# Performance work log

Hardware: AMD Instinct MI355X
Metric: run time of the kernel (lower is better)

Reference implementation:

```python
import jax, jax.numpy as jnp
import numpy as np

K = 1024          # num_embeddings
D = 64            # embedding_dim
TEMP = 1.0        # cfg.temperature
EPS = 1e-10


def setup_inputs() -> dict:
    key = jax.random.key(0)
    k1, k2 = jax.random.split(key)
    return {
        "inputs": jax.random.normal(k1, (16, 2048, D), dtype=jnp.float32),
        "embedding": jax.random.normal(k2, (K, D), dtype=jnp.float32),
        "code_count": jnp.ones((K,), dtype=jnp.float32),
    }


def _distances(flat, embedding):
    return ((flat ** 2).sum(axis=1, keepdims=True)
            + (embedding ** 2).sum(axis=1)
            - 2.0 * flat @ embedding.T)


def reference(inputs, embedding, code_count):
    B = inputs.shape[0]
    flat = inputs.reshape(-1, D)                      # [N, D]
    N = flat.shape[0]

    d = _distances(flat, embedding)                   # [N, K]
    idx = jnp.argmin(d, axis=1)                       # [N]

    # one-hot @ codebook == gather by index
    quantized = embedding[idx].reshape(inputs.shape)

    commitment_loss = jnp.mean((jax.lax.stop_gradient(quantized) - inputs) ** 2)

    # ortho loss over used codes (code_count >= 1), via masking (jit-safe)
    mask = (code_count >= 1.0).astype(inputs.dtype)   # [K]
    n_used = mask.sum()
    normed = embedding / jnp.clip(
        jnp.linalg.norm(embedding, axis=1, keepdims=True), 1e-12)
    normed = normed * mask[:, None]                   # zero out unused rows
    cos = normed @ normed.T                           # [K, K]
    ortho_loss = (cos ** 2).sum() / (n_used ** 2) - 1.0 / n_used

    # entropy loss over softmax(-d / T)
    prob = jax.nn.softmax(-d / TEMP, axis=1)          # [N, K]
    entropy_loss = -jnp.mean(jnp.sum(prob * jnp.log(prob + EPS), axis=1))
    entropy_loss = entropy_loss / jnp.log2(jnp.asarray(K, inputs.dtype))

    # straight-through estimator
    quantized_st = inputs + jax.lax.stop_gradient(quantized - inputs)

    # perplexity from code usage histogram (mean of one-hot encodings)
    avg_probs = jnp.zeros((K,), inputs.dtype).at[idx].add(1.0) / N
    perplexity = jnp.exp(-jnp.sum(avg_probs * jnp.log(avg_probs + EPS)))

    coverage = mask.sum() / K
    indices = idx.reshape(B, -1)

    return (quantized_st, commitment_loss, ortho_loss, entropy_loss,
            perplexity, coverage, indices)
```

## Files before the change

### kernel.cpp

```cpp
#include <hip/hip_runtime.h>
#include <math.h>

#define N_ROWS  32768
#define K_CODES 1024
#define D_DIM   64
#define NSPLIT  4
#define C_SHIFT 30.0f
#define LOG2E_F 1.4426950408889634f
#define LN2_F   0.6931471805599453f

#define WS_HIST   0
#define WS_ACC_H  1024
#define WS_ACC_C  1025
#define WS_NUSED  1026
#define WS_G      2048
#define WS_E2C    6144
#define PART_STRIDE (NSPLIT * N_ROWS)
#define WS_PART_S  8192
#define WS_PART_U  (8192 + PART_STRIDE)
#define WS_PART_AB (8192 + 2 * PART_STRIDE)
#define WS_EB      (8192 + 3 * PART_STRIDE)
#define CHUNK_F4  260
#define MAIN_CHUNKS 16
#define MEMSET_BYTES (6144 * 4)

#define OUT_Q      0
#define OUT_COMMIT 2097152
#define OUT_ORTHO  2097153
#define OUT_ENT    2097154
#define OUT_PERP   2097155
#define OUT_COV    2097156
#define OUT_IDX    2097157

typedef __attribute__((ext_vector_type(8))) _Float16 f16x8;
typedef __attribute__((ext_vector_type(4))) float f32x4;

__device__ inline float exact_g(const float4* X, const float* __restrict__ emb,
                                int k, float e2ck) {
    const float4* e4 = (const float4*)(emb + (size_t)k * D_DIM);
    float d0 = 0.f, d1 = 0.f, d2 = 0.f, d3 = 0.f;
#pragma unroll
    for (int j = 0; j < 16; j += 4) {
        float4 ea = e4[j], eb = e4[j + 1], ec = e4[j + 2], ed = e4[j + 3];
        float4 xa = X[j], xb = X[j + 1], xc = X[j + 2], xd = X[j + 3];
        d0 = fmaf(ea.x, xa.x, d0); d0 = fmaf(ea.y, xa.y, d0);
        d0 = fmaf(ea.z, xa.z, d0); d0 = fmaf(ea.w, xa.w, d0);
        d1 = fmaf(eb.x, xb.x, d1); d1 = fmaf(eb.y, xb.y, d1);
        d1 = fmaf(eb.z, xb.z, d1); d1 = fmaf(eb.w, xb.w, d1);
        d2 = fmaf(ec.x, xc.x, d2); d2 = fmaf(ec.y, xc.y, d2);
        d2 = fmaf(ec.z, xc.z, d2); d2 = fmaf(ec.w, xc.w, d2);
        d3 = fmaf(ed.x, xd.x, d3); d3 = fmaf(ed.y, xd.y, d3);
        d3 = fmaf(ed.z, xd.z, d3); d3 = fmaf(ed.w, xd.w, d3);
    }
    return fmaf(2.0f, (d0 + d1) + (d2 + d3), -e2ck);
}

__device__ inline void decomp2x8(const float* v, f16x8& h, f16x8& m) {
#pragma unroll
    for (int i = 0; i < 8; ++i) {
        _Float16 hh = (_Float16)v[i];
        h[i] = hh;
        m[i] = (_Float16)(v[i] - (float)hh);
    }
}

__global__ __launch_bounds__(256) void vq_prep_ortho(const float* __restrict__ emb,
                                                     const float* __restrict__ cc,
                                                     float* __restrict__ ws) {
    __shared__ float srows[64][64];
    __shared__ float rn2[64];
    const int t = threadIdx.x;

    if (blockIdx.x < 16) {
        const int tid  = blockIdx.x * 256 + t;
        const int c    = tid >> 6;
        const int lane = tid & 63;
        const int col  = lane & 15;
        const int kg   = lane >> 4;
        const int code = c * 16 + col;
        float4* EB4 = (float4*)(ws + WS_EB);
#pragma unroll
        for (int s = 0; s < 2; ++s) {
            const float* ep = emb + (size_t)code * D_DIM + s * 32 + kg * 8;
            float4 A4 = *(const float4*)ep;
            float4 B4 = *(const float4*)(ep + 4);
            float v[8] = {A4.x, A4.y, A4.z, A4.w, B4.x, B4.y, B4.z, B4.w};
            union { f16x8 h; float4 f; } th, tm;
            decomp2x8(v, th.h, tm.h);
            const int base = c * CHUNK_F4;
            EB4[base + (s * 2 + 0) * 64 + lane] = th.f;
            EB4[base + (s * 2 + 1) * 64 + lane] = tm.f;
        }
        if (kg == 0) {
            const float4* e4 = (const float4*)(emb + (size_t)code * D_DIM);
            float ssum = 0.f;
#pragma unroll
            for (int j = 0; j < 16; ++j) {
                float4 v = e4[j];
                ssum += v.x * v.x + v.y * v.y + v.z * v.z + v.w * v.w;
            }
            float e2c = ssum + C_SHIFT;
            ws[WS_E2C + code] = e2c;
            ((float*)(EB4 + c * CHUNK_F4 + 256))[col] = e2c * LOG2E_F;
            if (cc[code] >= 1.0f) atomicAdd(&ws[WS_NUSED], 1.0f);
        }
        return;
    }

    const int k0 = (blockIdx.x - 16) * 64;
    const int rb = t >> 4;
    const int c4 = (t & 15) << 2;

#pragma unroll
    for (int i = 0; i < 4; ++i) {
        const int r = i * 16 + rb;
        float4 v = *(const float4*)(emb + (size_t)(k0 + r) * D_DIM + c4);
        *(float4*)(&srows[r][c4]) = v;
        float ss = v.x * v.x + v.y * v.y + v.z * v.z + v.w * v.w;
        ss += __shfl_down(ss, 8, 16);
        ss += __shfl_down(ss, 4, 16);
        ss += __shfl_down(ss, 2, 16);
        ss += __shfl_down(ss, 1, 16);
        if ((t & 15) == 0) {
            float nrm = fmaxf(sqrtf(ss), 1e-12f);
            float m = (cc[k0 + r] >= 1.0f) ? 1.0f : 0.0f;
            rn2[r] = m / (nrm * nrm);
        }
    }
    __syncthreads();

    const int a  = t >> 2;
    const int b0 = (t & 3) << 4;
    float acc[16];
#pragma unroll
    for (int i = 0; i < 16; ++i) acc[i] = 0.f;

#pragma unroll 4
    for (int k = 0; k < 64; ++k) {
        float na = srows[k][a] * rn2[k];
        const float* rbp = &srows[k][b0];
#pragma unroll
        for (int i = 0; i < 16; ++i) acc[i] = fmaf(na, rbp[i], acc[i]);
    }
#pragma unroll
    for (int i = 0; i < 16; ++i)
        atomicAdd(&ws[WS_G + a * 64 + b0 + i], acc[i]);
}

#define MFMA_F16 __builtin_amdgcn_mfma_f32_16x16x32_f16

__global__ __launch_bounds__(256)
__attribute__((amdgpu_waves_per_eu(4, 4)))
void vq_main(const float* __restrict__ inp, float* __restrict__ ws) {
    const int t    = threadIdx.x;
    const int lane = t & 63;
    const int wave = t >> 6;
    const int col  = lane & 15;
    const int kg   = lane >> 4;
    const int rg   = blockIdx.x >> 2;
    const int sp   = blockIdx.x & 3;
    const int wbase = rg * 128 + wave * 32;

    f16x8 xa[2][4];
#pragma unroll
    for (int tt = 0; tt < 2; ++tt) {
        const float* xp = inp + (size_t)(wbase + tt * 16 + col) * D_DIM + kg * 8;
#pragma unroll
        for (int s = 0; s < 2; ++s) {
            float4 A4 = *(const float4*)(xp + s * 32);
            float4 B4 = *(const float4*)(xp + s * 32 + 4);
            float v[8] = {A4.x, A4.y, A4.z, A4.w, B4.x, B4.y, B4.z, B4.w};
            decomp2x8(v, xa[tt][s * 2 + 0], xa[tt][s * 2 + 1]);
        }
    }

    const float4* EBp = (const float4*)(ws + WS_EB)
                      + (size_t)sp * MAIN_CHUNKS * CHUNK_F4;

    float sa[2][4], ua[2][4], m1[2][4], m2[2][4];
    int i12[2][4];
#pragma unroll
    for (int tt = 0; tt < 2; ++tt)
#pragma unroll
        for (int q = 0; q < 4; ++q) {
            sa[tt][q] = 0.f; ua[tt][q] = 0.f;
            m1[tt][q] = -1e30f; m2[tt][q] = -1e30f;
            i12[tt][q] = 0;
        }

#pragma unroll 2
    for (int c = 0; c < MAIN_CHUNKS; ++c) {
        const float4* p = EBp + (size_t)c * CHUNK_F4;
        const f16x8* pb = (const f16x8*)p;
        f16x8 bh0 = pb[0 * 64 + lane];
        f16x8 bm0 = pb[1 * 64 + lane];
        f16x8 bh1 = pb[2 * 64 + lane];
        f16x8 bm1 = pb[3 * 64 + lane];
        const float e2v = ((const float*)(p + 256))[col];

        f32x4 acc[2];
#pragma unroll
        for (int tt = 0; tt < 2; ++tt) acc[tt] = (f32x4){0.f, 0.f, 0.f, 0.f};

#pragma unroll
        for (int tt = 0; tt < 2; ++tt) acc[tt] = MFMA_F16(xa[tt][0], bh0, acc[tt], 0, 0, 0);
#pragma unroll
        for (int tt = 0; tt < 2; ++tt) acc[tt] = MFMA_F16(xa[tt][2], bh1, acc[tt], 0, 0, 0);
#pragma unroll
        for (int tt = 0; tt < 2; ++tt) acc[tt] = MFMA_F16(xa[tt][1], bh0, acc[tt], 0, 0, 0);
#pragma unroll
        for (int tt = 0; tt < 2; ++tt) acc[tt] = MFMA_F16(xa[tt][3], bh1, acc[tt], 0, 0, 0);
#pragma unroll
        for (int tt = 0; tt < 2; ++tt) acc[tt] = MFMA_F16(xa[tt][0], bm0, acc[tt], 0, 0, 0);
#pragma unroll
        for (int tt = 0; tt < 2; ++tt) acc[tt] = MFMA_F16(xa[tt][2], bm1, acc[tt], 0, 0, 0);
#pragma unroll
        for (int tt = 0; tt < 2; ++tt) acc[tt] = MFMA_F16(xa[tt][1], bm0, acc[tt], 0, 0, 0);
#pragma unroll
        for (int tt = 0; tt < 2; ++tt) acc[tt] = MFMA_F16(xa[tt][3], bm1, acc[tt], 0, 0, 0);

        const int cb = sp * 256 + c * 16 + col;
#pragma unroll
        for (int tt = 0; tt < 2; ++tt)
#pragma unroll
            for (int q = 0; q < 4; ++q) {
                float g = fmaf(2.0f * LOG2E_F, acc[tt][q], -e2v);
                float pw;
                asm("v_exp_f32 %0, %1" : "=v"(pw) : "v"(g));
                sa[tt][q] += pw;
                ua[tt][q] = fmaf(pw, g, ua[tt][q]);
                bool gt1 = g > m1[tt][q];
                bool gt2 = g > m2[tt][q];
                int t1 = (cb << 10) | (i12[tt][q] >> 10);
                int t2 = (i12[tt][q] & ~1023) | cb;
                i12[tt][q] = gt1 ? t1 : (gt2 ? t2 : i12[tt][q]);
                m2[tt][q] = __builtin_amdgcn_fmed3f(g, m2[tt][q], m1[tt][q]);
                m1[tt][q] = fmaxf(m1[tt][q], g);
            }
    }

#pragma unroll
    for (int off = 1; off < 16; off <<= 1) {
#pragma unroll
        for (int tt = 0; tt < 2; ++tt)
#pragma unroll
            for (int q = 0; q < 4; ++q) {
                sa[tt][q] += __shfl_xor(sa[tt][q], off);
                ua[tt][q] += __shfl_xor(ua[tt][q], off);
                float bm1v = __shfl_xor(m1[tt][q], off);
                float bm2v = __shfl_xor(m2[tt][q], off);
                int   biv  = __shfl_xor(i12[tt][q], off);
                if (bm1v > m1[tt][q]) {
                    if (bm2v > m1[tt][q]) {
                        m2[tt][q] = bm2v; i12[tt][q] = biv;
                    } else {
                        m2[tt][q] = m1[tt][q];
                        i12[tt][q] = (biv & ~1023 & 0xFFFFFC00) | (i12[tt][q] >> 10);
                        i12[tt][q] = ((biv >> 10) << 10) | (i12[tt][q] & 1023);
                    }
                    m1[tt][q] = bm1v;
                } else if (bm1v > m2[tt][q]) {
                    m2[tt][q] = bm1v;
                    i12[tt][q] = (i12[tt][q] & ~1023) | (biv >> 10);
                }
            }
    }

    if (col == 0) {
#pragma unroll
        for (int tt = 0; tt < 2; ++tt)
#pragma unroll
            for (int q = 0; q < 4; ++q) {
                const int r  = wbase + tt * 16 + kg * 4 + q;
                const int pi = sp * N_ROWS + r;
                ws[WS_PART_S + pi]  = sa[tt][q];
                ws[WS_PART_U + pi]  = ua[tt][q];
                ws[WS_PART_AB + pi] = (float)i12[tt][q];
            }
    }
}

__global__ __launch_bounds__(64) void vq_combine(const float* __restrict__ inp,
                                                 const float* __restrict__ emb,
                                                 float* __restrict__ ws,
                                                 float* __restrict__ out) {
    const int lane = threadIdx.x;
    const int row  = blockIdx.x * 64 + lane;

    float S = 0.f, U2 = 0.f;
    int cand[8];
#pragma unroll
    for (int sp = 0; sp < NSPLIT; ++sp) {
        const int pi = sp * N_ROWS + row;
        S  += ws[WS_PART_S + pi];
        U2 += ws[WS_PART_U + pi];
        int ab = (int)ws[WS_PART_AB + pi];
        cand[2 * sp]     = ab >> 10;
        cand[2 * sp + 1] = ab & 1023;
    }
    float U = U2 * LN2_F;

    float4 X[16];
    const float4* xr = (const float4*)(inp + (size_t)row * D_DIM);
#pragma unroll
    for (int j = 0; j < 16; ++j) X[j] = xr[j];

    float bestg = -1e30f; int I = K_CODES;
#pragma unroll 2
    for (int j = 0; j < 8; ++j) {
        const int c = cand[j];
        float g = exact_g(X, emb, c, ws[WS_E2C + c]);
        if (g > bestg || (g == bestg && c < I)) { bestg = g; I = c; }
    }

    float H = logf(S) - U / S;

    out[OUT_IDX + row] = (float)I;
    atomicAdd(&ws[WS_HIST + I], 1.0f);

    const float4* q4 = (const float4*)(emb + (size_t)I * D_DIM);
    float4* oq = (float4*)out + (size_t)row * 16;
    float cs = 0.f;
#pragma unroll
    for (int j = 0; j < 16; ++j) {
        float4 q = q4[j], x = X[j];
        float dx = q.x - x.x, dy = q.y - x.y, dz = q.z - x.z, dw = q.w - x.w;
        cs += dx * dx + dy * dy + dz * dz + dw * dw;
        float4 o;
        o.x = x.x + dx; o.y = x.y + dy; o.z = x.z + dz; o.w = x.w + dw;
        oq[j] = o;
    }
#pragma unroll
    for (int off = 32; off; off >>= 1) {
        H  += __shfl_down(H, off);
        cs += __shfl_down(cs, off);
    }
    if (lane == 0) {
        atomicAdd(&ws[WS_ACC_H], H);
        atomicAdd(&ws[WS_ACC_C], cs);
    }
}

__global__ __launch_bounds__(256) void vq_finalize(const float* __restrict__ ws,
                                                   float* __restrict__ out) {
    __shared__ float redP[4], redG[4];
    const int t = threadIdx.x;
    float hp = 0.f, gg = 0.f;
    for (int k = t; k < K_CODES; k += 256) {
        float p = ws[WS_HIST + k] * (1.0f / (float)N_ROWS);
        hp += p * logf(p + 1e-10f);
    }
    for (int i = t; i < 4096; i += 256) {
        float g = ws[WS_G + i];
        gg = fmaf(g, g, gg);
    }
#pragma unroll
    for (int off = 32; off; off >>= 1) {
        hp += __shfl_down(hp, off);
        gg += __shfl_down(gg, off);
    }
    if ((t & 63) == 0) { redP[t >> 6] = hp; redG[t >> 6] = gg; }
    __syncthreads();
    if (t == 0) {
        float hsum = redP[0] + redP[1] + redP[2] + redP[3];
        float gsum = redG[0] + redG[1] + redG[2] + redG[3];
        float nu = ws[WS_NUSED];
        out[OUT_PERP]   = expf(-hsum);
        out[OUT_ENT]    = ws[WS_ACC_H] * (1.0f / (float)N_ROWS) * 0.1f;
        out[OUT_COMMIT] = ws[WS_ACC_C] * (1.0f / ((float)N_ROWS * (float)D_DIM));
        out[OUT_ORTHO]  = gsum / (nu * nu) - 1.0f / nu;
        out[OUT_COV]    = nu * (1.0f / (float)K_CODES);
    }
}

extern "C" void kernel_launch(void* const* d_in, const int* in_sizes, int n_in,
                              void* d_out, int out_size, void* d_ws, size_t ws_size,
                              hipStream_t stream) {
    const float* inp = (const float*)d_in[0];
    const float* emb = (const float*)d_in[1];
    const float* cc  = (const float*)d_in[2];
    float* out = (float*)d_out;
    float* ws  = (float*)d_ws;

    hipMemsetAsync(d_ws, 0, MEMSET_BYTES, stream);
    vq_prep_ortho<<<32, 256, 0, stream>>>(emb, cc, ws);
    vq_main<<<(N_ROWS / 128) * NSPLIT, 256, 0, stream>>>(inp, ws);
    vq_combine<<<N_ROWS / 64, 64, 0, stream>>>(inp, emb, ws, out);
    vq_finalize<<<1, 256, 0, stream>>>(ws, out);
}
```

Measured before the change: 148.3 us.

## Fold finalize into last combine block, drop memset, retile main to 16 rows per wave

Removes the memset and the separate finalize launch. Workspace counters are zeroed inside the prep kernel, and the last combine block, found through an atomic ticket, does the final reductions. The Gram-matrix atomics become per-block partial stores that are summed at the end, and the used-code count moves to that final step. The main kernel now gives each wave 16 rows instead of 32, doubles the grid and drops the waves_per_eu hint. This lowers register pressure but doubles codebook fragment loads per MFMA.

```diff
diff --git a/kernel.cpp b/kernel.cpp
--- a/kernel.cpp
+++ b/kernel.cpp
@@ -12,17 +12,16 @@
 #define WS_HIST   0
 #define WS_ACC_H  1024
 #define WS_ACC_C  1025
-#define WS_NUSED  1026
-#define WS_G      2048
+#define WS_CNT    1027
 #define WS_E2C    6144
 #define PART_STRIDE (NSPLIT * N_ROWS)
 #define WS_PART_S  8192
 #define WS_PART_U  (8192 + PART_STRIDE)
 #define WS_PART_AB (8192 + 2 * PART_STRIDE)
 #define WS_EB      (8192 + 3 * PART_STRIDE)
+#define WS_GP      467968
 #define CHUNK_F4  260
 #define MAIN_CHUNKS 16
-#define MEMSET_BYTES (6144 * 4)
 
 #define OUT_Q      0
 #define OUT_COMMIT 2097152
@@ -72,6 +71,9 @@
     const int t = threadIdx.x;
 
     if (blockIdx.x < 16) {
+        if (blockIdx.x < 4) ws[WS_HIST + blockIdx.x * 256 + t] = 0.f;
+        if (blockIdx.x == 0 && t < 4) ws[WS_ACC_H + t] = 0.f;
+
         const int tid  = blockIdx.x * 256 + t;
         const int c    = tid >> 6;
         const int lane = tid & 63;
@@ -102,12 +104,12 @@
             float e2c = ssum + C_SHIFT;
             ws[WS_E2C + code] = e2c;
             ((float*)(EB4 + c * CHUNK_F4 + 256))[col] = e2c * LOG2E_F;
-            if (cc[code] >= 1.0f) atomicAdd(&ws[WS_NUSED], 1.0f);
         }
         return;
     }
 
-    const int k0 = (blockIdx.x - 16) * 64;
+    const int ob = blockIdx.x - 16;
+    const int k0 = ob * 64;
     const int rb = t >> 4;
     const int c4 = (t & 15) << 2;
 
@@ -144,13 +146,12 @@
     }
 #pragma unroll
     for (int i = 0; i < 16; ++i)
-        atomicAdd(&ws[WS_G + a * 64 + b0 + i], acc[i]);
+        ws[WS_GP + ob * 4096 + a * 64 + b0 + i] = acc[i];
 }
 
 #define MFMA_F16 __builtin_amdgcn_mfma_f32_16x16x32_f16
 
 __global__ __launch_bounds__(256)
-__attribute__((amdgpu_waves_per_eu(4, 4)))
 void vq_main(const float* __restrict__ inp, float* __restrict__ ws) {
     const int t    = threadIdx.x;
     const int lane = t & 63;
@@ -159,36 +160,34 @@
     const int kg   = lane >> 4;
     const int rg   = blockIdx.x >> 2;
     const int sp   = blockIdx.x & 3;
-    const int wbase = rg * 128 + wave * 32;
-
-    f16x8 xa[2][4];
-#pragma unroll
-    for (int tt = 0; tt < 2; ++tt) {
-        const float* xp = inp + (size_t)(wbase + tt * 16 + col) * D_DIM + kg * 8;
-#pragma unroll
-        for (int s = 0; s < 2; ++s) {
-            float4 A4 = *(const float4*)(xp + s * 32);
-            float4 B4 = *(const float4*)(xp + s * 32 + 4);
-            float v[8] = {A4.x, A4.y, A4.z, A4.w, B4.x, B4.y, B4.z, B4.w};
-            decomp2x8(v, xa[tt][s * 2 + 0], xa[tt][s * 2 + 1]);
-        }
+    const int row  = rg * 64 + wave * 16 + col;
+
+    f16x8 xh0, xm0, xh1, xm1;
+    {
+        const float* xp = inp + (size_t)row * D_DIM + kg * 8;
+        float4 A4 = *(const float4*)xp;
+        float4 B4 = *(const float4*)(xp + 4);
+        float v[8] = {A4.x, A4.y, A4.z, A4.w, B4.x, B4.y, B4.z, B4.w};
+        decomp2x8(v, xh0, xm0);
+        A4 = *(const float4*)(xp + 32);
+        B4 = *(const float4*)(xp + 36);
+        float w[8] = {A4.x, A4.y, A4.z, A4.w, B4.x, B4.y, B4.z, B4.w};
+        decomp2x8(w, xh1, xm1);
     }
 
     const float4* EBp = (const float4*)(ws + WS_EB)
                       + (size_t)sp * MAIN_CHUNKS * CHUNK_F4;
 
-    float sa[2][4], ua[2][4], m1[2][4], m2[2][4];
-    int i12[2][4];
-#pragma unroll
-    for (int tt = 0; tt < 2; ++tt)
-#pragma unroll
-        for (int q = 0; q < 4; ++q) {
-            sa[tt][q] = 0.f; ua[tt][q] = 0.f;
-            m1[tt][q] = -1e30f; m2[tt][q] = -1e30f;
-            i12[tt][q] = 0;
-        }
-
-#pragma unroll 2
+    float sa[4], ua[4], m1[4], m2[4];
+    int i12[4];
+#pragma unroll
+    for (int q = 0; q < 4; ++q) {
+        sa[q] = 0.f; ua[q] = 0.f;
+        m1[q] = -1e30f; m2[q] = -1e30f;
+        i12[q] = 0;
+    }
+
+#pragma unroll 1
     for (int c = 0; c < MAIN_CHUNKS; ++c) {
         const float4* p = EBp + (size_t)c * CHUNK_F4;
         const f16x8* pb = (const f16x8*)p;
@@ -198,90 +197,74 @@
         f16x8 bm1 = pb[3 * 64 + lane];
         const float e2v = ((const float*)(p + 256))[col];
 
-        f32x4 acc[2];
-#pragma unroll
-        for (int tt = 0; tt < 2; ++tt) acc[tt] = (f32x4){0.f, 0.f, 0.f, 0.f};
-
-#pragma unroll
-        for (int tt = 0; tt < 2; ++tt) acc[tt] = MFMA_F16(xa[tt][0], bh0, acc[tt], 0, 0, 0);
-#pragma unroll
-        for (int tt = 0; tt < 2; ++tt) acc[tt] = MFMA_F16(xa[tt][2], bh1, acc[tt], 0, 0, 0);
-#pragma unroll
-        for (int tt = 0; tt < 2; ++tt) acc[tt] = MFMA_F16(xa[tt][1], bh0, acc[tt], 0, 0, 0);
-#pragma unroll
-        for (int tt = 0; tt < 2; ++tt) acc[tt] = MFMA_F16(xa[tt][3], bh1, acc[tt], 0, 0, 0);
-#pragma unroll
-        for (int tt = 0; tt < 2; ++tt) acc[tt] = MFMA_F16(xa[tt][0], bm0, acc[tt], 0, 0, 0);
-#pragma unroll
-        for (int tt = 0; tt < 2; ++tt) acc[tt] = MFMA_F16(xa[tt][2], bm1, acc[tt], 0, 0, 0);
-#pragma unroll
-        for (int tt = 0; tt < 2; ++tt) acc[tt] = MFMA_F16(xa[tt][1], bm0, acc[tt], 0, 0, 0);
-#pragma unroll
-        for (int tt = 0; tt < 2; ++tt) acc[tt] = MFMA_F16(xa[tt][3], bm1, acc[tt], 0, 0, 0);
+        f32x4 acc = {0.f, 0.f, 0.f, 0.f};
+        acc = MFMA_F16(xh0, bh0, acc, 0, 0, 0);
+        acc = MFMA_F16(xh1, bh1, acc, 0, 0, 0);
+        acc = MFMA_F16(xm0, bh0, acc, 0, 0, 0);
+        acc = MFMA_F16(xm1, bh1, acc, 0, 0, 0);
+        acc = MFMA_F16(xh0, bm0, acc, 0, 0, 0);
+        acc = MFMA_F16(xh1, bm1, acc, 0, 0, 0);
+        acc = MFMA_F16(xm0, bm0, acc, 0, 0, 0);
+        acc = MFMA_F16(xm1, bm1, acc, 0, 0, 0);
 
         const int cb = sp * 256 + c * 16 + col;
 #pragma unroll
-        for (int tt = 0; tt < 2; ++tt)
-#pragma unroll
-            for (int q = 0; q < 4; ++q) {
-                float g = fmaf(2.0f * LOG2E_F, acc[tt][q], -e2v);
-                float pw;
-                asm("v_exp_f32 %0, %1" : "=v"(pw) : "v"(g));
-                sa[tt][q] += pw;
-                ua[tt][q] = fmaf(pw, g, ua[tt][q]);
-                bool gt1 = g > m1[tt][q];
-                bool gt2 = g > m2[tt][q];
-                int t1 = (cb << 10) | (i12[tt][q] >> 10);
-                int t2 = (i12[tt][q] & ~1023) | cb;
-                i12[tt][q] = gt1 ? t1 : (gt2 ? t2 : i12[tt][q]);
-                m2[tt][q] = __builtin_amdgcn_fmed3f(g, m2[tt][q], m1[tt][q]);
-                m1[tt][q] = fmaxf(m1[tt][q], g);
+        for (int q = 0; q < 4; ++q) {
+            float g = fmaf(2.0f * LOG2E_F, acc[q], -e2v);
+            float pw;
+            asm("v_exp_f32 %0, %1" : "=v"(pw) : "v"(g));
+            sa[q] += pw;
+            ua[q] = fmaf(pw, g, ua[q]);
+            bool gt1 = g > m1[q];
+            bool gt2 = g > m2[q];
+            int t1 = (cb << 10) | (i12[q] >> 10);
+            int t2 = (i12[q] & ~1023) | cb;
+            i12[q] = gt1 ? t1 : (gt2 ? t2 : i12[q]);
+            m2[q] = __builtin_amdgcn_fmed3f(g, m2[q], m1[q]);
+            m1[q] = fmaxf(m1[q], g);
+        }
+    }
+
+#pragma unroll
+    for (int off = 1; off < 16; off <<= 1) {
+#pragma unroll
+        for (int q = 0; q < 4; ++q) {
+            sa[q] += __shfl_xor(sa[q], off);
+            ua[q] += __shfl_xor(ua[q], off);
+            float bm1v = __shfl_xor(m1[q], off);
+            float bm2v = __shfl_xor(m2[q], off);
+            int   biv  = __shfl_xor(i12[q], off);
+            if (bm1v > m1[q]) {
+                if (bm2v > m1[q]) {
+                    m2[q] = bm2v; i12[q] = biv;
+                } else {
+                    m2[q] = m1[q];
+                    i12[q] = (biv & ~1023 & 0xFFFFFC00) | (i12[q] >> 10);
+                    i12[q] = ((biv >> 10) << 10) | (i12[q] & 1023);
+                }
+                m1[q] = bm1v;
+            } else if (bm1v > m2[q]) {
+                m2[q] = bm1v;
+                i12[q] = (i12[q] & ~1023) | (biv >> 10);
             }
-    }
-
-#pragma unroll
-    for (int off = 1; off < 16; off <<= 1) {
-#pragma unroll
-        for (int tt = 0; tt < 2; ++tt)
-#pragma unroll
-            for (int q = 0; q < 4; ++q) {
-                sa[tt][q] += __shfl_xor(sa[tt][q], off);
-                ua[tt][q] += __shfl_xor(ua[tt][q], off);
-                float bm1v = __shfl_xor(m1[tt][q], off);
-                float bm2v = __shfl_xor(m2[tt][q], off);
-                int   biv  = __shfl_xor(i12[tt][q], off);
-                if (bm1v > m1[tt][q]) {
-                    if (bm2v > m1[tt][q]) {
-                        m2[tt][q] = bm2v; i12[tt][q] = biv;
-                    } else {
-                        m2[tt][q] = m1[tt][q];
-                        i12[tt][q] = (biv & ~1023 & 0xFFFFFC00) | (i12[tt][q] >> 10);
-                        i12[tt][q] = ((biv >> 10) << 10) | (i12[tt][q] & 1023);
-                    }
-                    m1[tt][q] = bm1v;
-                } else if (bm1v > m2[tt][q]) {
-                    m2[tt][q] = bm1v;
-                    i12[tt][q] = (i12[tt][q] & ~1023) | (biv >> 10);
-                }
-            }
+        }
     }
 
     if (col == 0) {
 #pragma unroll
-        for (int tt = 0; tt < 2; ++tt)
-#pragma unroll
-            for (int q = 0; q < 4; ++q) {
-                const int r  = wbase + tt * 16 + kg * 4 + q;
-                const int pi = sp * N_ROWS + r;
-                ws[WS_PART_S + pi]  = sa[tt][q];
-                ws[WS_PART_U + pi]  = ua[tt][q];
-                ws[WS_PART_AB + pi] = (float)i12[tt][q];
-            }
+        for (int q = 0; q < 4; ++q) {
+            const int r  = rg * 64 + wave * 16 + kg * 4 + q;
+            const int pi = sp * N_ROWS + r;
+            ws[WS_PART_S + pi]  = sa[q];
+            ws[WS_PART_U + pi]  = ua[q];
+            ws[WS_PART_AB + pi] = (float)i12[q];
+        }
     }
 }
 
 __global__ __launch_bounds__(64) void vq_combine(const float* __restrict__ inp,
                                                  const float* __restrict__ emb,
+                                                 const float* __restrict__ cc,
                                                  float* __restrict__ ws,
                                                  float* __restrict__ out) {
     const int lane = threadIdx.x;
@@ -339,36 +322,45 @@
         atomicAdd(&ws[WS_ACC_H], H);
         atomicAdd(&ws[WS_ACC_C], cs);
     }
-}
-
-__global__ __launch_bounds__(256) void vq_finalize(const float* __restrict__ ws,
-                                                   float* __restrict__ out) {
-    __shared__ float redP[4], redG[4];
-    const int t = threadIdx.x;
-    float hp = 0.f, gg = 0.f;
-    for (int k = t; k < K_CODES; k += 256) {
-        float p = ws[WS_HIST + k] * (1.0f / (float)N_ROWS);
+
+    __threadfence();
+    int old = 0;
+    if (lane == 0) old = atomicAdd((int*)ws + WS_CNT, 1);
+    old = __shfl(old, 0);
+    if (old != 511) return;
+
+    float hp = 0.f, gg = 0.f, nu = 0.f;
+    for (int k = lane; k < K_CODES; k += 64) {
+        float h = __hip_atomic_load(ws + WS_HIST + k, __ATOMIC_RELAXED,
+                                    __HIP_MEMORY_SCOPE_AGENT);
+        float p = h * (1.0f / (float)N_ROWS);
         hp += p * logf(p + 1e-10f);
-    }
-    for (int i = t; i < 4096; i += 256) {
-        float g = ws[WS_G + i];
-        gg = fmaf(g, g, gg);
+        nu += (cc[k] >= 1.0f) ? 1.0f : 0.0f;
+    }
+    for (int i4 = lane; i4 < 1024; i4 += 64) {
+        float4 s = {0.f, 0.f, 0.f, 0.f};
+#pragma unroll 4
+        for (int b = 0; b < 16; ++b) {
+            float4 v = *(const float4*)(ws + WS_GP + b * 4096 + i4 * 4);
+            s.x += v.x; s.y += v.y; s.z += v.z; s.w += v.w;
+        }
+        gg += s.x * s.x + s.y * s.y + s.z * s.z + s.w * s.w;
     }
 #pragma unroll
     for (int off = 32; off; off >>= 1) {
         hp += __shfl_down(hp, off);
         gg += __shfl_down(gg, off);
-    }
-    if ((t & 63) == 0) { redP[t >> 6] = hp; redG[t >> 6] = gg; }
-    __syncthreads();
-    if (t == 0) {
-        float hsum = redP[0] + redP[1] + redP[2] + redP[3];
-        float gsum = redG[0] + redG[1] + redG[2] + redG[3];
-        float nu = ws[WS_NUSED];
-        out[OUT_PERP]   = expf(-hsum);
-        out[OUT_ENT]    = ws[WS_ACC_H] * (1.0f / (float)N_ROWS) * 0.1f;
-        out[OUT_COMMIT] = ws[WS_ACC_C] * (1.0f / ((float)N_ROWS * (float)D_DIM));
-        out[OUT_ORTHO]  = gsum / (nu * nu) - 1.0f / nu;
+        nu += __shfl_down(nu, off);
+    }
+    if (lane == 0) {
+        float H2 = __hip_atomic_load(ws + WS_ACC_H, __ATOMIC_RELAXED,
+                                     __HIP_MEMORY_SCOPE_AGENT);
+        float C2 = __hip_atomic_load(ws + WS_ACC_C, __ATOMIC_RELAXED,
+                                     __HIP_MEMORY_SCOPE_AGENT);
+        out[OUT_PERP]   = expf(-hp);
+        out[OUT_ENT]    = H2 * (1.0f / (float)N_ROWS) * 0.1f;
+        out[OUT_COMMIT] = C2 * (1.0f / ((float)N_ROWS * (float)D_DIM));
+        out[OUT_ORTHO]  = gg / (nu * nu) - 1.0f / nu;
         out[OUT_COV]    = nu * (1.0f / (float)K_CODES);
     }
 }
@@ -382,9 +374,7 @@
     float* out = (float*)d_out;
     float* ws  = (float*)d_ws;
 
-    hipMemsetAsync(d_ws, 0, MEMSET_BYTES, stream);
     vq_prep_ortho<<<32, 256, 0, stream>>>(emb, cc, ws);
-    vq_main<<<(N_ROWS / 128) * NSPLIT, 256, 0, stream>>>(inp, ws);
-    vq_combine<<<N_ROWS / 64, 64, 0, stream>>>(inp, emb, ws, out);
-    vq_finalize<<<1, 256, 0, stream>>>(ws, out);
-}
+    vq_main<<<(N_ROWS / 64) * NSPLIT, 256, 0, stream>>>(inp, ws);
+    vq_combine<<<N_ROWS / 64, 64, 0, stream>>>(inp, emb, cc, ws, out);
+}
```

After: 187.5 us. +26.4%, slower.
